# Kernel tuning notes

Measured on AMD Instinct MI355X. Metric: run time of the kernel, lower is better.

## Reference

```python
import jax, jax.numpy as jnp
import numpy as np

B, S, D = 1, 2048, 2048      # batch, seq, hidden_dim
DF = 768                      # moe intermediate (per routed expert)
DSH = 2048                    # shared-expert intermediate
E, K = 32, 8                  # num routed experts, top_k
BLK = 128                     # fp8 block-scale size
CAP = 1024
T = B * S


def _dequant(w, s, blk=BLK):
    # w: [E, M, N] fp8 values (stored fp32), s: [E, M/blk, N/blk] block scales
    Eh, M, N = w.shape
    Mb, Nb = s.shape[1], s.shape[2]
    return (w.reshape(Eh, Mb, blk, Nb, blk) * s[:, :, None, :, None]).reshape(Eh, M, N)


def setup_inputs() -> dict:
    key = jax.random.key(0)
    ks = jax.random.split(key, 13)
    n = lambda k, shp, sc=0.02: jax.random.normal(k, shp, jnp.float32) * sc
    u = lambda k, shp: jax.random.uniform(k, shp, jnp.float32, 0.005, 0.02)
    return {
        "hidden_states": jax.random.normal(ks[0], (B, S, D), jnp.float32),
        "router_w": n(ks[1], (E, D)),
        # raw fp8-value weights (simulated as fp32 integers-in-range values) + block scale_inv
        "wg_fp8": jax.random.normal(ks[2], (E, DF, D), jnp.float32),
        "sg": u(ks[3], (E, DF // BLK, D // BLK)),
        "wu_fp8": jax.random.normal(ks[4], (E, DF, D), jnp.float32),
        "su": u(ks[5], (E, DF // BLK, D // BLK)),
        "wd_fp8": jax.random.normal(ks[6], (E, D, DF), jnp.float32),
        "sd": u(ks[7], (E, D // BLK, DF // BLK)),
        "ws_gate": n(ks[8], (DSH, D)),
        "ws_up": n(ks[9], (DSH, D)),
        "ws_down": n(ks[10], (D, DSH)),
        "w_shared_gate": n(ks[11], (1, D)),
    }


def reference(hidden_states, router_w, wg_fp8, sg, wu_fp8, su, wd_fp8, sd,
              ws_gate, ws_up, ws_down, w_shared_gate):
    x = hidden_states.reshape(-1, D)  # [T, D]

    # shared expert (SwiGLU) + its sigmoid gate
    shared = (jax.nn.silu(x @ ws_gate.T) * (x @ ws_up.T)) @ ws_down.T
    sh_gate = jax.nn.sigmoid(x @ w_shared_gate.T)  # [T, 1]

    # router: softmax -> top-k -> renormalize (Qwen MoE gate)
    probs = jax.nn.softmax(x @ router_w.T, axis=-1)          # [T, E]
    rw, sel = jax.lax.top_k(probs, K)                        # [T, K]
    rw = rw / jnp.sum(rw, axis=-1, keepdims=True)

    # capacity-based dispatch (replaces the python per-expert loop; same math)
    flat_e = sel.reshape(-1)                                 # [T*K]
    oh = jax.nn.one_hot(flat_e, E, dtype=jnp.int32)
    pos = jnp.sum(jnp.cumsum(oh, axis=0) * oh, axis=-1) - 1  # position within expert
    keep = (pos < CAP)
    pos_c = jnp.minimum(pos, CAP)                            # overflow -> scratch slot CAP
    tok = jnp.arange(T * K) // K                             # owning token of each (t,k) pair

    buf = jnp.zeros((E, CAP + 1, D), x.dtype).at[flat_e, pos_c].set(x[tok])

    # block-scale dequant (fp8*scale_inv), then per-expert SwiGLU
    Wg = _dequant(wg_fp8, sg)
    Wu = _dequant(wu_fp8, su)
    Wd = _dequant(wd_fp8, sd)
    g = jnp.einsum('ecd,efd->ecf', buf, Wg)
    up = jnp.einsum('ecd,efd->ecf', buf, Wu)
    h = jax.nn.silu(g) * up
    y = jnp.einsum('ecf,edf->ecd', h, Wd)                    # [E, CAP+1, D]

    # weighted scatter-add back to tokens (index_add_ equivalent)
    y_tok = y[flat_e, pos_c]                                 # [T*K, D]
    w_tok = rw.reshape(-1) * keep.astype(x.dtype)
    out = jax.ops.segment_sum(y_tok * w_tok[:, None], tok, num_segments=T)

    out = out + sh_gate * shared
    return out.reshape(B, S, D)
```

## Files before the change

### kernel.cpp

```cpp
#include <hip/hip_runtime.h>
#include <hip/hip_bf16.h>


#define TT   2048
#define DD   2048
#define DFF  768
#define DSH  2048
#define EE   32
#define KTOP 8
#define CAP  1024

typedef _Float16 half8  __attribute__((ext_vector_type(8)));
typedef _Float16 half4v __attribute__((ext_vector_type(4)));
typedef float    f32x4  __attribute__((ext_vector_type(4)));

__global__ __launch_bounds__(256) void k_init(int* __restrict__ cnt,
                                              int* __restrict__ slot_tok) {
  int i = blockIdx.x * 256 + threadIdx.x;
  if (i < EE * CAP) slot_tok[i] = 0;
  if (i < EE) cnt[i] = 0;
}

__global__ __launch_bounds__(256) void k_cast(const float* __restrict__ in,
                                              _Float16* __restrict__ out) {
  int i = blockIdx.x * 256 + threadIdx.x;
  float4 v = ((const float4*)in)[i];
  half4v h = { (_Float16)v.x, (_Float16)v.y, (_Float16)v.z, (_Float16)v.w };
  ((half4v*)out)[i] = h;
}

template<int NCOLS>
__global__ void k_deq_row(const float* __restrict__ w, const float* __restrict__ s,
                          int mRows, _Float16* __restrict__ outp) {
  int r = blockIdx.x, e = blockIdx.y;
  int c4 = threadIdx.x;
  long long base = ((long long)e * mRows + r) * NCOLS;
  float sc = s[(e * (mRows >> 7) + (r >> 7)) * (NCOLS >> 7) + (c4 >> 5)];
  float4 v = ((const float4*)(w + base))[c4];
  half4v h = { (_Float16)(v.x * sc), (_Float16)(v.y * sc),
               (_Float16)(v.z * sc), (_Float16)(v.w * sc) };
  ((half4v*)(outp + base))[c4] = h;
}

__global__ __launch_bounds__(64) void k_router(
    const float* __restrict__ x, const float* __restrict__ rw,
    const float* __restrict__ wshg,
    float* __restrict__ shg, int* __restrict__ cnt,
    int* __restrict__ slot_tok, float* __restrict__ slot_w,
    int* __restrict__ slot_pair, int* __restrict__ pair_pos) {
  int t = blockIdx.x;
  int lane = threadIdx.x;
  const float* xr = x + (size_t)t * DD;
  float xv[32];
#pragma unroll
  for (int j = 0; j < 32; ++j) xv[j] = xr[lane + j * 64];

  __shared__ float lg[EE];
  for (int e = 0; e < EE; ++e) {
    const float* we = rw + (size_t)e * DD;
    float s = 0.f;
#pragma unroll
    for (int j = 0; j < 32; ++j) s += xv[j] * we[lane + j * 64];
#pragma unroll
    for (int off = 32; off > 0; off >>= 1) s += __shfl_down(s, off);
    if (lane == 0) lg[e] = s;
  }
  {
    float s = 0.f;
#pragma unroll
    for (int j = 0; j < 32; ++j) s += xv[j] * wshg[lane + j * 64];
#pragma unroll
    for (int off = 32; off > 0; off >>= 1) s += __shfl_down(s, off);
    if (lane == 0) shg[t] = 1.f / (1.f + expf(-s));
  }
  if (lane == 0) {
    unsigned used = 0;
    int sel[KTOP];
    float val[KTOP];
    for (int k = 0; k < KTOP; ++k) {
      float bv = -1e30f; int bi = 0;
      for (int e = 0; e < EE; ++e)
        if (!((used >> e) & 1) && lg[e] > bv) { bv = lg[e]; bi = e; }
      used |= (1u << bi);
      sel[k] = bi; val[k] = bv;
    }
    float mx = val[0], sum = 0.f;
    for (int k = 0; k < KTOP; ++k) { val[k] = expf(val[k] - mx); sum += val[k]; }
    float inv = 1.f / sum;
    for (int k = 0; k < KTOP; ++k) {
      int e = sel[k];
      int pos = atomicAdd(&cnt[e], 1);
      pair_pos[t * KTOP + k] = pos;
      if (pos < CAP) {
        slot_tok[e * CAP + pos] = t;
        slot_w[e * CAP + pos] = val[k] * inv;
        slot_pair[e * CAP + pos] = t * KTOP + k;
      }
    }
  }
}

template<bool DUAL, bool GATHER, int EPI, int NPB, int MBB, int KDIM>
__global__ __launch_bounds__(256, 2) void k_gemm16(
    const _Float16* __restrict__ A,
    const _Float16* __restrict__ B0h, const _Float16* __restrict__ B1h,
    _Float16* __restrict__ OutH, float* __restrict__ OutF,
    const float* __restrict__ shg,
    int ldA, int ldOut,
    long long strideAE, long long strideBE, long long strideOE,
    const int* __restrict__ cnt, int rowsConst,
    const int* __restrict__ slot_tok, const float* __restrict__ slot_w) {
  constexpr int BK = 64;
  constexpr int KT = KDIM / BK;
  constexpr int NF = DUAL ? 2 : 4;
  constexpr int BN = DUAL ? 64 : 128;

  const int f = blockIdx.x;
  const int xcd = f & 7;
  const int t0 = f >> 3;
  const int mb = t0 % MBB;
  const int pp = t0 / MBB;
  const int p  = pp * 8 + xcd;
  const int nb = p % NPB;
  const int e  = p / NPB;

  int rows = cnt ? (cnt[e] > CAP ? CAP : cnt[e]) : rowsConst;
  const int rowBase = mb * 128;
  if (rowBase >= rows) return;
  const int nBase = nb * BN;

  const int tid = threadIdx.x;
  const int lane = tid & 63;
  const int wave = tid >> 6;
  const int wr = wave >> 1;
  const int wc = wave & 1;

  __shared__ __align__(16) _Float16 sA[3][8192];
  __shared__ __align__(16) _Float16 sB[2][8192];

  const _Float16* Ae = A + (GATHER ? 0 : (long long)e * strideAE);
  const _Float16* B0e = B0h + (long long)e * strideBE;
  const _Float16* B1e = DUAL ? (B1h + (long long)e * strideBE) : nullptr;

  int aByte[4];
#pragma unroll
  for (int i = 0; i < 4; ++i) {
    int c = tid + i * 256;
    int row = c >> 3;
    int colB = ((c & 7) << 4) ^ ((row & 7) << 4);
    int src = GATHER ? slot_tok[e * CAP + rowBase + row] : (rowBase + row);
    aByte[i] = src * (2 * ldA) + colB;
  }
  int bByte[4];
#pragma unroll
  for (int i = 0; i < 4; ++i) {
    int c = tid + i * 256;
    int rn = DUAL ? ((c & 511) >> 3) : (c >> 3);
    int colB = ((c & 7) << 4) ^ ((rn & 7) << 4);
    bByte[i] = (nBase + rn) * (2 * KDIM) + colB;
  }

  f32x4 accG[4][NF];
  f32x4 accU[DUAL ? 4 : 1][NF];
#pragma unroll
  for (int m = 0; m < 4; ++m)
#pragma unroll
    for (int n = 0; n < NF; ++n) {
      accG[m][n] = (f32x4){0.f, 0.f, 0.f, 0.f};
      if constexpr (DUAL) accU[m][n] = (f32x4){0.f, 0.f, 0.f, 0.f};
    }

  auto stageA = [&](int kt, int buf) {
#pragma unroll
    for (int i = 0; i < 4; ++i) {
      __builtin_amdgcn_global_load_lds(
          (const __attribute__((address_space(1))) void*)
              ((const char*)Ae + aByte[i] + kt * 128),
          (__attribute__((address_space(3))) void*)&sA[buf][(tid + i * 256) * 8],
          16, 0, 0);
    }
  };
  auto stageB = [&](int kt, int buf) {
#pragma unroll
    for (int i = 0; i < 4; ++i) {
      const _Float16* src = (DUAL && i >= 2) ? B1e : B0e;
      __builtin_amdgcn_global_load_lds(
          (const __attribute__((address_space(1))) void*)
              ((const char*)src + bByte[i] + kt * 128),
          (__attribute__((address_space(3))) void*)&sB[buf][(tid + i * 256) * 8],
          16, 0, 0);
    }
  };
  auto computeTile = [&](int ia, int ib) {
    const char* pA = (const char*)&sA[ia][0];
    const char* pB = (const char*)&sB[ib][0];
#pragma unroll
    for (int kk = 0; kk < 2; ++kk) {
      const int koff = kk * 32 + (lane >> 4) * 8;
      half8 a[4];
#pragma unroll
      for (int m = 0; m < 4; ++m) {
        int r = wr * 64 + m * 16 + (lane & 15);
        int byt = ((r << 7) + (koff << 1)) ^ ((r & 7) << 4);
        a[m] = *(const half8*)(pA + byt);
      }
      if constexpr (DUAL) {
        half8 bg[2], bu[2];
#pragma unroll
        for (int n = 0; n < 2; ++n) {
          int rn = wc * 32 + n * 16 + (lane & 15);
          int byt = ((rn << 7) + (koff << 1)) ^ ((rn & 7) << 4);
          bg[n] = *(const half8*)(pB + byt);
          bu[n] = *(const half8*)(pB + 8192 + byt);
        }
#pragma unroll
        for (int m = 0; m < 4; ++m)
#pragma unroll
          for (int n = 0; n < 2; ++n) {
            accG[m][n] = __builtin_amdgcn_mfma_f32_16x16x32_f16(a[m], bg[n], accG[m][n], 0, 0, 0);
            accU[m][n] = __builtin_amdgcn_mfma_f32_16x16x32_f16(a[m], bu[n], accU[m][n], 0, 0, 0);
          }
      } else {
        half8 b[4];
#pragma unroll
        for (int n = 0; n < 4; ++n) {
          int rn = wc * 64 + n * 16 + (lane & 15);
          int byt = ((rn << 7) + (koff << 1)) ^ ((rn & 7) << 4);
          b[n] = *(const half8*)(pB + byt);
        }
#pragma unroll
        for (int m = 0; m < 4; ++m)
#pragma unroll
          for (int n = 0; n < 4; ++n)
            accG[m][n] = __builtin_amdgcn_mfma_f32_16x16x32_f16(a[m], b[n], accG[m][n], 0, 0, 0);
      }
    }
  };

  stageB(0, 0);
  __builtin_amdgcn_sched_barrier(0);
  stageA(0, 0);
  __builtin_amdgcn_sched_barrier(0);
  stageA(1, 1);
  __builtin_amdgcn_sched_barrier(0);

  int bufC = 0, bufW = 2;
  for (int kt = 0; kt < KT; ++kt) {
    asm volatile("s_waitcnt lgkmcnt(0)" ::: "memory");
    if (kt + 1 < KT) { asm volatile("s_waitcnt vmcnt(4)" ::: "memory"); }
    else             { asm volatile("s_waitcnt vmcnt(0)" ::: "memory"); }
    __builtin_amdgcn_sched_barrier(0);
    __builtin_amdgcn_s_barrier();
    __builtin_amdgcn_sched_barrier(0);
    if (kt + 1 < KT) stageB(kt + 1, (kt + 1) & 1);
    if (kt + 2 < KT) stageA(kt + 2, bufW);
    __builtin_amdgcn_sched_barrier(0);
    computeTile(bufC, kt & 1);
    bufC = (bufC == 2) ? 0 : bufC + 1;
    bufW = (bufW == 2) ? 0 : bufW + 1;
  }

#pragma unroll
  for (int m = 0; m < 4; ++m) {
#pragma unroll
    for (int i = 0; i < 4; ++i) {
      int row = rowBase + wr * 64 + m * 16 + (lane >> 4) * 4 + i;
      if (row < rows) {
        if constexpr (EPI == 1) {
          int pair = slot_tok[e * CAP + row];
          float w = slot_w[e * CAP + row];
#pragma unroll
          for (int n = 0; n < NF; ++n) {
            int col = nBase + wc * 64 + n * 16 + (lane & 15);
            OutH[(long long)pair * DD + col] = (_Float16)(w * accG[m][n][i]);
          }
        } else if constexpr (EPI == 2) {
          float g = shg[row];
#pragma unroll
          for (int n = 0; n < NF; ++n) {
            int col = nBase + wc * 64 + n * 16 + (lane & 15);
            OutF[(long long)row * DD + col] += g * accG[m][n][i];
          }
        } else {
          long long outBase = (long long)e * strideOE;
#pragma unroll
          for (int n = 0; n < NF; ++n) {
            int col = nBase + (DUAL ? wc * 32 : wc * 64) + n * 16 + (lane & 15);
            long long o = outBase + (long long)row * ldOut + col;
            if constexpr (DUAL) {
              float gv = accG[m][n][i];
              float uv = accU[m][n][i];
              OutH[o] = (_Float16)((gv / (1.f + __expf(-gv))) * uv);
            } else {
              OutH[o] = (_Float16)accG[m][n][i];
            }
          }
        }
      }
    }
  }
}

template<bool DUAL, bool GATHER, bool DEQ, int EPI, int NPB, int MBB, int KDIM>
__global__ __launch_bounds__(256, 2) void k_gemm(
    const _Float16* __restrict__ A,
    const float* __restrict__ B0f, const float* __restrict__ B1f,
    const float* __restrict__ S0, const float* __restrict__ S1,
    int sCols, int sStrideE,
    _Float16* __restrict__ OutH, float* __restrict__ OutF,
    const float* __restrict__ shg,
    int ldA, int ldOut,
    long long strideAE, long long strideBE, long long strideOE,
    const int* __restrict__ cnt, int rowsConst,
    const int* __restrict__ slot_tok, const float* __restrict__ slot_w) {
  constexpr int BK = 64;
  constexpr int KT = KDIM / BK;
  constexpr int NF = DUAL ? 2 : 4;
  constexpr int BN = DUAL ? 64 : 128;
  constexpr int BCH = DUAL ? 4 : 8;

  const int f = blockIdx.x;
  const int xcd = f & 7;
  const int t0 = f >> 3;
  const int mb = t0 % MBB;
  const int pp = t0 / MBB;
  const int p  = pp * 8 + xcd;
  const int nb = p % NPB;
  const int e  = p / NPB;

  int rows = cnt ? (cnt[e] > CAP ? CAP : cnt[e]) : rowsConst;
  const int rowBase = mb * 128;
  if (rowBase >= rows) return;
  const int nBase = nb * BN;

  const int tid = threadIdx.x;
  const int lane = tid & 63;
  const int wave = tid >> 6;
  const int wr = wave >> 1;
  const int wc = wave & 1;

  __shared__ __align__(16) _Float16 sA[3][8192];
  __shared__ __align__(16) _Float16 sB[2][8192];

  const _Float16* Ae = A + (GATHER ? 0 : (long long)e * strideAE);
  const float* B0e = B0f + (long long)e * strideBE;
  const float* B1e = DUAL ? (B1f + (long long)e * strideBE) : nullptr;
  const float* S0e = DEQ ? (S0 + (long long)e * sStrideE) : nullptr;
  const float* S1e = (DEQ && DUAL) ? (S1 + (long long)e * sStrideE) : nullptr;
  const int sRow = DEQ ? (nBase >> 7) * sCols : 0;

  int aByte[4];
#pragma unroll
  for (int i = 0; i < 4; ++i) {
    int c = tid + i * 256;
    int row = c >> 3;
    int colB = ((c & 7) << 4) ^ ((row & 7) << 4);
    int src = GATHER ? slot_tok[e * CAP + rowBase + row] : (rowBase + row);
    aByte[i] = src * (2 * ldA) + colB;
  }
  int bOff[BCH], wByte[BCH];
#pragma unroll
  for (int i = 0; i < BCH; ++i) {
    int c = tid + i * 256;
    int rn = c >> 4;
    int c4 = (c & 15) << 2;
    bOff[i] = (nBase + rn) * KDIM + c4;
    wByte[i] = ((rn << 7) + (c4 << 1)) ^ ((rn & 7) << 4);
  }

  f32x4 accG[4][NF];
  f32x4 accU[DUAL ? 4 : 1][NF];
#pragma unroll
  for (int m = 0; m < 4; ++m)
#pragma unroll
    for (int n = 0; n < NF; ++n) {
      accG[m][n] = (f32x4){0.f, 0.f, 0.f, 0.f};
      if constexpr (DUAL) accU[m][n] = (f32x4){0.f, 0.f, 0.f, 0.f};
    }

  auto stageA = [&](int kt, int buf) {
#pragma unroll
    for (int i = 0; i < 4; ++i) {
      __builtin_amdgcn_global_load_lds(
          (const __attribute__((address_space(1))) void*)
              ((const char*)Ae + aByte[i] + kt * (BK * 2)),
          (__attribute__((address_space(3))) void*)&sA[buf][(tid + i * 256) * 8],
          16, 0, 0);
    }
  };
  auto loadB = [&](int kt, float4 (&r0)[BCH], float4 (&r1)[BCH]) {
    const int ko = kt * BK;
#pragma unroll
    for (int i = 0; i < BCH; ++i) r0[i] = *(const float4*)(B0e + bOff[i] + ko);
    if constexpr (DUAL) {
#pragma unroll
      for (int i = 0; i < BCH; ++i) r1[i] = *(const float4*)(B1e + bOff[i] + ko);
    }
  };
  auto storeB = [&](int kt, float4 (&r0)[BCH], float4 (&r1)[BCH]) {
    float s0 = 1.f, s1 = 1.f;
    if constexpr (DEQ) {
      s0 = S0e[sRow + (kt >> 1)];
      if constexpr (DUAL) s1 = S1e[sRow + (kt >> 1)];
    }
    char* base = (char*)&sB[kt & 1][0];
#pragma unroll
    for (int i = 0; i < BCH; ++i) {
      half4v h = { (_Float16)(r0[i].x * s0), (_Float16)(r0[i].y * s0),
                   (_Float16)(r0[i].z * s0), (_Float16)(r0[i].w * s0) };
      *(half4v*)(base + wByte[i]) = h;
      if constexpr (DUAL) {
        half4v h1 = { (_Float16)(r1[i].x * s1), (_Float16)(r1[i].y * s1),
                      (_Float16)(r1[i].z * s1), (_Float16)(r1[i].w * s1) };
        *(half4v*)(base + 8192 + wByte[i]) = h1;
      }
    }
  };
  auto computeTile = [&](int ia, int ib) {
    const char* pA = (const char*)&sA[ia][0];
    const char* pB = (const char*)&sB[ib][0];
#pragma unroll
    for (int kk = 0; kk < 2; ++kk) {
      const int koff = kk * 32 + (lane >> 4) * 8;
      half8 a[4];
#pragma unroll
      for (int m = 0; m < 4; ++m) {
        int r = wr * 64 + m * 16 + (lane & 15);
        int byt = ((r << 7) + (koff << 1)) ^ ((r & 7) << 4);
        a[m] = *(const half8*)(pA + byt);
      }
      if constexpr (DUAL) {
        half8 bg[2], bu[2];
#pragma unroll
        for (int n = 0; n < 2; ++n) {
          int rn = wc * 32 + n * 16 + (lane & 15);
          int byt = ((rn << 7) + (koff << 1)) ^ ((rn & 7) << 4);
          bg[n] = *(const half8*)(pB + byt);
          bu[n] = *(const half8*)(pB + 8192 + byt);
        }
#pragma unroll
        for (int m = 0; m < 4; ++m)
#pragma unroll
          for (int n = 0; n < 2; ++n) {
            accG[m][n] = __builtin_amdgcn_mfma_f32_16x16x32_f16(a[m], bg[n], accG[m][n], 0, 0, 0);
            accU[m][n] = __builtin_amdgcn_mfma_f32_16x16x32_f16(a[m], bu[n], accU[m][n], 0, 0, 0);
          }
      } else {
        half8 b[4];
#pragma unroll
        for (int n = 0; n < 4; ++n) {
          int rn = wc * 64 + n * 16 + (lane & 15);
          int byt = ((rn << 7) + (koff << 1)) ^ ((rn & 7) << 4);
          b[n] = *(const half8*)(pB + byt);
        }
#pragma unroll
        for (int m = 0; m < 4; ++m)
#pragma unroll
          for (int n = 0; n < 4; ++n)
            accG[m][n] = __builtin_amdgcn_mfma_f32_16x16x32_f16(a[m], b[n], accG[m][n], 0, 0, 0);
      }
    }
  };

  float4 rbE0[BCH], rbE1[BCH], rbO0[BCH], rbO1[BCH];

  stageA(0, 0); loadB(0, rbE0, rbE1);
  __builtin_amdgcn_sched_barrier(0);
  stageA(1, 1); loadB(1, rbO0, rbO1);
  __builtin_amdgcn_sched_barrier(0);

  int bufC = 0, bufW = 2;

  for (int kt = 0; kt < KT; kt += 2) {
    if (kt + 1 < KT) { asm volatile("s_waitcnt vmcnt(12)" ::: "memory"); }
    else             { asm volatile("s_waitcnt vmcnt(0)"  ::: "memory"); }
    __builtin_amdgcn_sched_barrier(0);
    storeB(kt, rbE0, rbE1);
    asm volatile("s_waitcnt lgkmcnt(0)" ::: "memory");
    __builtin_amdgcn_sched_barrier(0);
    __builtin_amdgcn_s_barrier();
    __builtin_amdgcn_sched_barrier(0);
    if (kt + 2 < KT) { stageA(kt + 2, bufW); loadB(kt + 2, rbE0, rbE1); }
    __builtin_amdgcn_sched_barrier(0);
    computeTile(bufC, 0);
    bufC = (bufC == 2) ? 0 : bufC + 1;
    bufW = (bufW == 2) ? 0 : bufW + 1;

    if (kt + 2 < KT) { asm volatile("s_waitcnt vmcnt(12)" ::: "memory"); }
    else             { asm volatile("s_waitcnt vmcnt(0)"  ::: "memory"); }
    __builtin_amdgcn_sched_barrier(0);
    storeB(kt + 1, rbO0, rbO1);
    asm volatile("s_waitcnt lgkmcnt(0)" ::: "memory");
    __builtin_amdgcn_sched_barrier(0);
    __builtin_amdgcn_s_barrier();
    __builtin_amdgcn_sched_barrier(0);
    if (kt + 3 < KT) { stageA(kt + 3, bufW); loadB(kt + 3, rbO0, rbO1); }
    __builtin_amdgcn_sched_barrier(0);
    computeTile(bufC, 1);
    bufC = (bufC == 2) ? 0 : bufC + 1;
    bufW = (bufW == 2) ? 0 : bufW + 1;
  }

#pragma unroll
  for (int m = 0; m < 4; ++m) {
#pragma unroll
    for (int i = 0; i < 4; ++i) {
      int row = rowBase + wr * 64 + m * 16 + (lane >> 4) * 4 + i;
      if (row < rows) {
        if constexpr (EPI == 1) {
          int pair = slot_tok[e * CAP + row];
          float w = slot_w[e * CAP + row];
#pragma unroll
          for (int n = 0; n < NF; ++n) {
            int col = nBase + wc * 64 + n * 16 + (lane & 15);
            OutH[(long long)pair * DD + col] = (_Float16)(w * accG[m][n][i]);
          }
        } else if constexpr (EPI == 2) {
          float g = shg[row];
#pragma unroll
          for (int n = 0; n < NF; ++n) {
            int col = nBase + wc * 64 + n * 16 + (lane & 15);
            OutF[(long long)row * DD + col] += g * accG[m][n][i];
          }
        } else {
          long long outBase = (long long)e * strideOE;
#pragma unroll
          for (int n = 0; n < NF; ++n) {
            int col = nBase + (DUAL ? wc * 32 : wc * 64) + n * 16 + (lane & 15);
            long long o = outBase + (long long)row * ldOut + col;
            if constexpr (DUAL) {
              float gv = accG[m][n][i];
              float uv = accU[m][n][i];
              OutH[o] = (_Float16)((gv / (1.f + __expf(-gv))) * uv);
            } else {
              OutH[o] = (_Float16)accG[m][n][i];
            }
          }
        }
      }
    }
  }
}

__global__ __launch_bounds__(256) void k_combine(
    const _Float16* __restrict__ Yp, const int* __restrict__ pair_pos,
    float* __restrict__ out) {
  int t = blockIdx.x;
  int col = threadIdx.x * 8;
  float acc[8] = {0.f, 0.f, 0.f, 0.f, 0.f, 0.f, 0.f, 0.f};
#pragma unroll
  for (int k = 0; k < KTOP; ++k) {
    if (pair_pos[t * KTOP + k] < CAP) {
      half8 y = *(const half8*)&Yp[((size_t)t * KTOP + k) * DD + col];
#pragma unroll
      for (int j = 0; j < 8; ++j) acc[j] += (float)y[j];
    }
  }
  float4 o0 = {acc[0], acc[1], acc[2], acc[3]};
  float4 o1 = {acc[4], acc[5], acc[6], acc[7]};
  *(float4*)&out[(size_t)t * DD + col] = o0;
  *(float4*)&out[(size_t)t * DD + col + 4] = o1;
}

extern "C" void kernel_launch(void* const* d_in, const int* in_sizes, int n_in,
                              void* d_out, int out_size, void* d_ws, size_t ws_size,
                              hipStream_t stream) {
  (void)in_sizes; (void)n_in; (void)out_size;
  const float* x    = (const float*)d_in[0];
  const float* rw   = (const float*)d_in[1];
  const float* wg   = (const float*)d_in[2];
  const float* sg   = (const float*)d_in[3];
  const float* wu   = (const float*)d_in[4];
  const float* su   = (const float*)d_in[5];
  const float* wd   = (const float*)d_in[6];
  const float* sd   = (const float*)d_in[7];
  const float* wsg  = (const float*)d_in[8];
  const float* wsu  = (const float*)d_in[9];
  const float* wsd  = (const float*)d_in[10];
  const float* wshg = (const float*)d_in[11];
  float* out = (float*)d_out;

  char* p = (char*)d_ws;
  auto alloc = [&](size_t bytes) {
    char* r = p;
    p += (bytes + 255) & ~(size_t)255;
    return r;
  };

  const bool big = ws_size >= (size_t)270 * 1000 * 1000;

  if (big) {
    _Float16* x_h  = (_Float16*)alloc((size_t)TT * DD * 2);
    _Float16* bufA = (_Float16*)alloc((size_t)EE * DFF * DD * 2);
    _Float16* bufB = (_Float16*)alloc((size_t)EE * DFF * DD * 2);
    _Float16* bufH = (_Float16*)alloc((size_t)EE * CAP * DFF * 2);
    _Float16* Hsh  = (_Float16*)alloc((size_t)TT * DSH * 2);
    float* shg     = (float*)alloc((size_t)TT * 4);
    int* cnt       = (int*)alloc((size_t)EE * 4);
    int* slot_tok  = (int*)alloc((size_t)EE * CAP * 4);
    float* slot_w  = (float*)alloc((size_t)EE * CAP * 4);
    int* slot_pair = (int*)alloc((size_t)EE * CAP * 4);
    int* pair_pos  = (int*)alloc((size_t)TT * KTOP * 4);

    _Float16* Yp    = bufB;
    _Float16* wsg_h = bufH;
    _Float16* wsu_h = bufH + (size_t)TT * DD;
    _Float16* wsd_h = bufH + (size_t)2 * TT * DD;

    k_init<<<(EE * CAP + 255) / 256, 256, 0, stream>>>(cnt, slot_tok);
    k_cast<<<(TT * DD / 4) / 256, 256, 0, stream>>>(x, x_h);
    k_router<<<TT, 64, 0, stream>>>(x, rw, wshg, shg, cnt, slot_tok, slot_w,
                                    slot_pair, pair_pos);

    k_deq_row<DD><<<dim3(DFF, EE), DD / 4, 0, stream>>>(wg, sg, DFF, bufA);
    k_deq_row<DD><<<dim3(DFF, EE), DD / 4, 0, stream>>>(wu, su, DFF, bufB);

    k_gemm16<true, true, 0, 12, 8, DD><<<3072, 256, 0, stream>>>(
        x_h, bufA, bufB, bufH, nullptr, nullptr,
        DD, DFF, 0LL, (long long)DFF * DD, (long long)CAP * DFF,
        cnt, 0, slot_tok, nullptr);

    k_deq_row<DFF><<<dim3(DD, EE), DFF / 4, 0, stream>>>(wd, sd, DD, bufA);
    k_gemm16<false, false, 1, 16, 8, DFF><<<4096, 256, 0, stream>>>(
        bufH, bufA, bufA, Yp, nullptr, nullptr,
        DFF, DD, (long long)CAP * DFF, (long long)DD * DFF, 0LL,
        cnt, 0, slot_pair, slot_w);

    k_combine<<<TT, 256, 0, stream>>>(Yp, pair_pos, out);

    k_cast<<<(DD * DSH / 4) / 256, 256, 0, stream>>>(wsg, wsg_h);
    k_cast<<<(DD * DSH / 4) / 256, 256, 0, stream>>>(wsu, wsu_h);
    k_cast<<<(DD * DSH / 4) / 256, 256, 0, stream>>>(wsd, wsd_h);

    k_gemm16<true, false, 0, 32, 16, DD><<<512, 256, 0, stream>>>(
        x_h, wsg_h, wsu_h, Hsh, nullptr, nullptr,
        DD, DSH, 0LL, 0LL, 0LL,
        nullptr, TT, nullptr, nullptr);

    k_gemm16<false, false, 2, 16, 16, DSH><<<256, 256, 0, stream>>>(
        Hsh, wsd_h, wsd_h, nullptr, out, shg,
        DSH, DD, 0LL, 0LL, 0LL,
        nullptr, TT, nullptr, nullptr);
  } else {
    _Float16* x_h   = (_Float16*)alloc((size_t)TT * DD * 2);
    _Float16* H     = (_Float16*)alloc((size_t)EE * CAP * DFF * 2);
    _Float16* Hsh   = (_Float16*)alloc((size_t)TT * DSH * 2);
    _Float16* Yp    = (_Float16*)alloc((size_t)TT * KTOP * DD * 2);
    float* shg      = (float*)alloc((size_t)TT * 4);
    int* cnt        = (int*)alloc((size_t)EE * 4);
    int* slot_tok   = (int*)alloc((size_t)EE * CAP * 4);
    float* slot_w   = (float*)alloc((size_t)EE * CAP * 4);
    int* slot_pair  = (int*)alloc((size_t)EE * CAP * 4);
    int* pair_pos   = (int*)alloc((size_t)TT * KTOP * 4);

    k_init<<<(EE * CAP + 255) / 256, 256, 0, stream>>>(cnt, slot_tok);
    k_cast<<<(TT * DD / 4) / 256, 256, 0, stream>>>(x, x_h);
    k_router<<<TT, 64, 0, stream>>>(x, rw, wshg, shg, cnt, slot_tok, slot_w,
                                    slot_pair, pair_pos);

    k_gemm<true, true, true, 0, 12, 8, DD><<<3072, 256, 0, stream>>>(
        x_h, wg, wu, sg, su, DD / 128, (DFF / 128) * (DD / 128),
        H, nullptr, nullptr,
        DD, DFF, 0LL, (long long)DFF * DD, (long long)CAP * DFF,
        cnt, 0, slot_tok, nullptr);

    k_gemm<false, false, true, 1, 16, 8, DFF><<<4096, 256, 0, stream>>>(
        H, wd, wd, sd, sd, DFF / 128, (DD / 128) * (DFF / 128),
        Yp, nullptr, nullptr,
        DFF, DD, (long long)CAP * DFF, (long long)DD * DFF, 0LL,
        cnt, 0, slot_pair, slot_w);

    k_combine<<<TT, 256, 0, stream>>>(Yp, pair_pos, out);

    k_gemm<true, false, false, 0, 32, 16, DD><<<512, 256, 0, stream>>>(
        x_h, wsg, wsu, nullptr, nullptr, 0, 0,
        Hsh, nullptr, nullptr,
        DD, DSH, 0LL, 0LL, 0LL,
        nullptr, TT, nullptr, nullptr);

    k_gemm<false, false, false, 2, 16, 16, DSH><<<256, 256, 0, stream>>>(
        Hsh, wsd, wsd, nullptr, nullptr, 0, 0,
        nullptr, out, shg,
        DSH, DD, 0LL, 0LL, 0LL,
        nullptr, TT, nullptr, nullptr);
  }
}
```

Before: 747.3 us.

## Fuse routed-expert weight dequant into GEMM and drop the precomputed-weight path

Removes the workspace-size switch and the separate dequant kernels that wrote fp16 copies of the expert weights. The routed-expert GEMMs now read fp32 fp8-valued weights and block scales directly, scaling and converting them in registers before writing to LDS. Shared-expert weights are always cast to fp16 up front and use the plain fp16 GEMM. This saves the full write and re-read of the dequantized expert weights. In exchange, each M-block re-reads fp32 weights and does the conversion inside the GEMM loop, which puts more pressure on L2 and registers.

```diff
diff --git a/kernel.cpp b/kernel.cpp
--- a/kernel.cpp
+++ b/kernel.cpp
@@ -27,19 +27,6 @@
   float4 v = ((const float4*)in)[i];
   half4v h = { (_Float16)v.x, (_Float16)v.y, (_Float16)v.z, (_Float16)v.w };
   ((half4v*)out)[i] = h;
-}
-
-template<int NCOLS>
-__global__ void k_deq_row(const float* __restrict__ w, const float* __restrict__ s,
-                          int mRows, _Float16* __restrict__ outp) {
-  int r = blockIdx.x, e = blockIdx.y;
-  int c4 = threadIdx.x;
-  long long base = ((long long)e * mRows + r) * NCOLS;
-  float sc = s[(e * (mRows >> 7) + (r >> 7)) * (NCOLS >> 7) + (c4 >> 5)];
-  float4 v = ((const float4*)(w + base))[c4];
-  half4v h = { (_Float16)(v.x * sc), (_Float16)(v.y * sc),
-               (_Float16)(v.z * sc), (_Float16)(v.w * sc) };
-  ((half4v*)(outp + base))[c4] = h;
 }
 
 __global__ __launch_bounds__(64) void k_router(
@@ -101,19 +88,21 @@
 }
 
 template<bool DUAL, bool GATHER, int EPI, int NPB, int MBB, int KDIM>
-__global__ __launch_bounds__(256, 2) void k_gemm16(
+__global__ __launch_bounds__(256, 2) void k_gemm(
     const _Float16* __restrict__ A,
-    const _Float16* __restrict__ B0h, const _Float16* __restrict__ B1h,
-    _Float16* __restrict__ OutH, float* __restrict__ OutF,
-    const float* __restrict__ shg,
+    const float* __restrict__ B0f, const float* __restrict__ B1f,
+    const float* __restrict__ S0, const float* __restrict__ S1,
+    int sCols, int sStrideE,
+    _Float16* __restrict__ OutH,
     int ldA, int ldOut,
     long long strideAE, long long strideBE, long long strideOE,
-    const int* __restrict__ cnt, int rowsConst,
+    const int* __restrict__ cnt,
     const int* __restrict__ slot_tok, const float* __restrict__ slot_w) {
   constexpr int BK = 64;
   constexpr int KT = KDIM / BK;
   constexpr int NF = DUAL ? 2 : 4;
   constexpr int BN = DUAL ? 64 : 128;
+  constexpr int BCH = DUAL ? 4 : 8;
 
   const int f = blockIdx.x;
   const int xcd = f & 7;
@@ -124,7 +113,7 @@
   const int nb = p % NPB;
   const int e  = p / NPB;
 
-  int rows = cnt ? (cnt[e] > CAP ? CAP : cnt[e]) : rowsConst;
+  int rows = cnt[e] > CAP ? CAP : cnt[e];
   const int rowBase = mb * 128;
   if (rowBase >= rows) return;
   const int nBase = nb * BN;
@@ -139,8 +128,11 @@
   __shared__ __align__(16) _Float16 sB[2][8192];
 
   const _Float16* Ae = A + (GATHER ? 0 : (long long)e * strideAE);
-  const _Float16* B0e = B0h + (long long)e * strideBE;
-  const _Float16* B1e = DUAL ? (B1h + (long long)e * strideBE) : nullptr;
+  const float* B0e = B0f + (long long)e * strideBE;
+  const float* B1e = DUAL ? (B1f + (long long)e * strideBE) : nullptr;
+  const float* S0e = S0 + (long long)e * sStrideE;
+  const float* S1e = DUAL ? (S1 + (long long)e * sStrideE) : nullptr;
+  const int sRow = (nBase >> 7) * sCols;
 
   int aByte[4];
 #pragma unroll
@@ -151,6 +143,218 @@
     int src = GATHER ? slot_tok[e * CAP + rowBase + row] : (rowBase + row);
     aByte[i] = src * (2 * ldA) + colB;
   }
+  int bOff[BCH], wByte[BCH];
+#pragma unroll
+  for (int i = 0; i < BCH; ++i) {
+    int c = tid + i * 256;
+    int rn = c >> 4;
+    int c4 = (c & 15) << 2;
+    bOff[i] = (nBase + rn) * KDIM + c4;
+    wByte[i] = ((rn << 7) + (c4 << 1)) ^ ((rn & 7) << 4);
+  }
+
+  f32x4 accG[4][NF];
+  f32x4 accU[DUAL ? 4 : 1][NF];
+#pragma unroll
+  for (int m = 0; m < 4; ++m)
+#pragma unroll
+    for (int n = 0; n < NF; ++n) {
+      accG[m][n] = (f32x4){0.f, 0.f, 0.f, 0.f};
+      if constexpr (DUAL) accU[m][n] = (f32x4){0.f, 0.f, 0.f, 0.f};
+    }
+
+  auto stageA = [&](int kt, int buf) {
+#pragma unroll
+    for (int i = 0; i < 4; ++i) {
+      __builtin_amdgcn_global_load_lds(
+          (const __attribute__((address_space(1))) void*)
+              ((const char*)Ae + aByte[i] + kt * (BK * 2)),
+          (__attribute__((address_space(3))) void*)&sA[buf][(tid + i * 256) * 8],
+          16, 0, 0);
+    }
+  };
+  auto loadB = [&](int kt, float4 (&r0)[BCH], float4 (&r1)[BCH]) {
+    const int ko = kt * BK;
+#pragma unroll
+    for (int i = 0; i < BCH; ++i) r0[i] = *(const float4*)(B0e + bOff[i] + ko);
+    if constexpr (DUAL) {
+#pragma unroll
+      for (int i = 0; i < BCH; ++i) r1[i] = *(const float4*)(B1e + bOff[i] + ko);
+    }
+  };
+  auto storeB = [&](int kt, float4 (&r0)[BCH], float4 (&r1)[BCH]) {
+    float s0 = S0e[sRow + (kt >> 1)];
+    float s1 = DUAL ? S1e[sRow + (kt >> 1)] : 0.f;
+    char* base = (char*)&sB[kt & 1][0];
+#pragma unroll
+    for (int i = 0; i < BCH; ++i) {
+      half4v h = { (_Float16)(r0[i].x * s0), (_Float16)(r0[i].y * s0),
+                   (_Float16)(r0[i].z * s0), (_Float16)(r0[i].w * s0) };
+      *(half4v*)(base + wByte[i]) = h;
+      if constexpr (DUAL) {
+        half4v h1 = { (_Float16)(r1[i].x * s1), (_Float16)(r1[i].y * s1),
+                      (_Float16)(r1[i].z * s1), (_Float16)(r1[i].w * s1) };
+        *(half4v*)(base + 8192 + wByte[i]) = h1;
+      }
+    }
+  };
+  auto computeTile = [&](int ia, int ib) {
+    const char* pA = (const char*)&sA[ia][0];
+    const char* pB = (const char*)&sB[ib][0];
+#pragma unroll
+    for (int kk = 0; kk < 2; ++kk) {
+      const int koff = kk * 32 + (lane >> 4) * 8;
+      half8 a[4];
+#pragma unroll
+      for (int m = 0; m < 4; ++m) {
+        int r = wr * 64 + m * 16 + (lane & 15);
+        int byt = ((r << 7) + (koff << 1)) ^ ((r & 7) << 4);
+        a[m] = *(const half8*)(pA + byt);
+      }
+      if constexpr (DUAL) {
+        half8 bg[2], bu[2];
+#pragma unroll
+        for (int n = 0; n < 2; ++n) {
+          int rn = wc * 32 + n * 16 + (lane & 15);
+          int byt = ((rn << 7) + (koff << 1)) ^ ((rn & 7) << 4);
+          bg[n] = *(const half8*)(pB + byt);
+          bu[n] = *(const half8*)(pB + 8192 + byt);
+        }
+#pragma unroll
+        for (int m = 0; m < 4; ++m)
+#pragma unroll
+          for (int n = 0; n < 2; ++n) {
+            accG[m][n] = __builtin_amdgcn_mfma_f32_16x16x32_f16(a[m], bg[n], accG[m][n], 0, 0, 0);
+            accU[m][n] = __builtin_amdgcn_mfma_f32_16x16x32_f16(a[m], bu[n], accU[m][n], 0, 0, 0);
+          }
+      } else {
+        half8 b[4];
+#pragma unroll
+        for (int n = 0; n < 4; ++n) {
+          int rn = wc * 64 + n * 16 + (lane & 15);
+          int byt = ((rn << 7) + (koff << 1)) ^ ((rn & 7) << 4);
+          b[n] = *(const half8*)(pB + byt);
+        }
+#pragma unroll
+        for (int m = 0; m < 4; ++m)
+#pragma unroll
+          for (int n = 0; n < 4; ++n)
+            accG[m][n] = __builtin_amdgcn_mfma_f32_16x16x32_f16(a[m], b[n], accG[m][n], 0, 0, 0);
+      }
+    }
+  };
+
+  float4 rbE0[BCH], rbE1[BCH], rbO0[BCH], rbO1[BCH];
+
+  loadB(0, rbE0, rbE1);
+  loadB(1, rbO0, rbO1);
+  stageA(0, 0);
+  stageA(1, 1);
+  __builtin_amdgcn_sched_barrier(0);
+  storeB(0, rbE0, rbE1);
+  asm volatile("s_waitcnt lgkmcnt(0)" ::: "memory");
+  asm volatile("s_waitcnt vmcnt(4)" ::: "memory");
+  __builtin_amdgcn_s_barrier();
+  __builtin_amdgcn_sched_barrier(0);
+
+  int bufC = 0, bufW = 2;
+  for (int kt = 0; kt < KT; ++kt) {
+    if (kt + 2 < KT) {
+      stageA(kt + 2, bufW);
+      if (kt & 1) loadB(kt + 2, rbO0, rbO1);
+      else        loadB(kt + 2, rbE0, rbE1);
+      __builtin_amdgcn_sched_barrier(0);
+    }
+    computeTile(bufC, kt & 1);
+    if (kt + 1 < KT) {
+      if (kt & 1) storeB(kt + 1, rbE0, rbE1);
+      else        storeB(kt + 1, rbO0, rbO1);
+    }
+    asm volatile("s_waitcnt lgkmcnt(0)" ::: "memory");
+    if (kt + 2 < KT) { asm volatile("s_waitcnt vmcnt(12)" ::: "memory"); }
+    else             { asm volatile("s_waitcnt vmcnt(0)"  ::: "memory"); }
+    __builtin_amdgcn_s_barrier();
+    __builtin_amdgcn_sched_barrier(0);
+    bufC = (bufC == 2) ? 0 : bufC + 1;
+    bufW = (bufW == 2) ? 0 : bufW + 1;
+  }
+
+#pragma unroll
+  for (int m = 0; m < 4; ++m) {
+#pragma unroll
+    for (int i = 0; i < 4; ++i) {
+      int row = rowBase + wr * 64 + m * 16 + (lane >> 4) * 4 + i;
+      if (row < rows) {
+        if constexpr (EPI == 1) {
+          int pair = slot_tok[e * CAP + row];
+          float w = slot_w[e * CAP + row];
+#pragma unroll
+          for (int n = 0; n < NF; ++n) {
+            int col = nBase + wc * 64 + n * 16 + (lane & 15);
+            OutH[(long long)pair * DD + col] = (_Float16)(w * accG[m][n][i]);
+          }
+        } else {
+          long long outBase = (long long)e * strideOE;
+#pragma unroll
+          for (int n = 0; n < NF; ++n) {
+            int col = nBase + (DUAL ? wc * 32 : wc * 64) + n * 16 + (lane & 15);
+            long long o = outBase + (long long)row * ldOut + col;
+            if constexpr (DUAL) {
+              float gv = accG[m][n][i];
+              float uv = accU[m][n][i];
+              OutH[o] = (_Float16)((gv / (1.f + __expf(-gv))) * uv);
+            } else {
+              OutH[o] = (_Float16)accG[m][n][i];
+            }
+          }
+        }
+      }
+    }
+  }
+}
+
+template<bool DUAL, int EPI, int NPB, int MBB, int KDIM>
+__global__ __launch_bounds__(256, 2) void k_gemm16(
+    const _Float16* __restrict__ A,
+    const _Float16* __restrict__ B0h, const _Float16* __restrict__ B1h,
+    _Float16* __restrict__ OutH, float* __restrict__ OutF,
+    const float* __restrict__ shg,
+    int ldA, int ldOut, int rowsConst) {
+  constexpr int BK = 64;
+  constexpr int KT = KDIM / BK;
+  constexpr int NF = DUAL ? 2 : 4;
+  constexpr int BN = DUAL ? 64 : 128;
+
+  const int f = blockIdx.x;
+  const int xcd = f & 7;
+  const int t0 = f >> 3;
+  const int mb = t0 % MBB;
+  const int pp = t0 / MBB;
+  const int p  = pp * 8 + xcd;
+  const int nb = p % NPB;
+
+  int rows = rowsConst;
+  const int rowBase = mb * 128;
+  if (rowBase >= rows) return;
+  const int nBase = nb * BN;
+
+  const int tid = threadIdx.x;
+  const int lane = tid & 63;
+  const int wave = tid >> 6;
+  const int wr = wave >> 1;
+  const int wc = wave & 1;
+
+  __shared__ __align__(16) _Float16 sA[3][8192];
+  __shared__ __align__(16) _Float16 sB[2][8192];
+
+  int aByte[4];
+#pragma unroll
+  for (int i = 0; i < 4; ++i) {
+    int c = tid + i * 256;
+    int row = c >> 3;
+    int colB = ((c & 7) << 4) ^ ((row & 7) << 4);
+    aByte[i] = (rowBase + row) * (2 * ldA) + colB;
+  }
   int bByte[4];
 #pragma unroll
   for (int i = 0; i < 4; ++i) {
@@ -175,7 +379,7 @@
     for (int i = 0; i < 4; ++i) {
       __builtin_amdgcn_global_load_lds(
           (const __attribute__((address_space(1))) void*)
-              ((const char*)Ae + aByte[i] + kt * 128),
+              ((const char*)A + aByte[i] + kt * 128),
           (__attribute__((address_space(3))) void*)&sA[buf][(tid + i * 256) * 8],
           16, 0, 0);
     }
@@ -183,7 +387,7 @@
   auto stageB = [&](int kt, int buf) {
 #pragma unroll
     for (int i = 0; i < 4; ++i) {
-      const _Float16* src = (DUAL && i >= 2) ? B1e : B0e;
+      const _Float16* src = (DUAL && i >= 2) ? B1h : B0h;
       __builtin_amdgcn_global_load_lds(
           (const __attribute__((address_space(1))) void*)
               ((const char*)src + bByte[i] + kt * 128),
@@ -266,15 +470,7 @@
     for (int i = 0; i < 4; ++i) {
       int row = rowBase + wr * 64 + m * 16 + (lane >> 4) * 4 + i;
       if (row < rows) {
-        if constexpr (EPI == 1) {
-          int pair = slot_tok[e * CAP + row];
-          float w = slot_w[e * CAP + row];
-#pragma unroll
-          for (int n = 0; n < NF; ++n) {
-            int col = nBase + wc * 64 + n * 16 + (lane & 15);
-            OutH[(long long)pair * DD + col] = (_Float16)(w * accG[m][n][i]);
-          }
-        } else if constexpr (EPI == 2) {
+        if constexpr (EPI == 2) {
           float g = shg[row];
 #pragma unroll
           for (int n = 0; n < NF; ++n) {
@@ -282,11 +478,10 @@
             OutF[(long long)row * DD + col] += g * accG[m][n][i];
           }
         } else {
-          long long outBase = (long long)e * strideOE;
 #pragma unroll
           for (int n = 0; n < NF; ++n) {
             int col = nBase + (DUAL ? wc * 32 : wc * 64) + n * 16 + (lane & 15);
-            long long o = outBase + (long long)row * ldOut + col;
+            long long o = (long long)row * ldOut + col;
             if constexpr (DUAL) {
               float gv = accG[m][n][i];
               float uv = accU[m][n][i];
@@ -301,247 +496,6 @@
   }
 }
 
-template<bool DUAL, bool GATHER, bool DEQ, int EPI, int NPB, int MBB, int KDIM>
-__global__ __launch_bounds__(256, 2) void k_gemm(
-    const _Float16* __restrict__ A,
-    const float* __restrict__ B0f, const float* __restrict__ B1f,
-    const float* __restrict__ S0, const float* __restrict__ S1,
-    int sCols, int sStrideE,
-    _Float16* __restrict__ OutH, float* __restrict__ OutF,
-    const float* __restrict__ shg,
-    int ldA, int ldOut,
-    long long strideAE, long long strideBE, long long strideOE,
-    const int* __restrict__ cnt, int rowsConst,
-    const int* __restrict__ slot_tok, const float* __restrict__ slot_w) {
-  constexpr int BK = 64;
-  constexpr int KT = KDIM / BK;
-  constexpr int NF = DUAL ? 2 : 4;
-  constexpr int BN = DUAL ? 64 : 128;
-  constexpr int BCH = DUAL ? 4 : 8;
-
-  const int f = blockIdx.x;
-  const int xcd = f & 7;
-  const int t0 = f >> 3;
-  const int mb = t0 % MBB;
-  const int pp = t0 / MBB;
-  const int p  = pp * 8 + xcd;
-  const int nb = p % NPB;
-  const int e  = p / NPB;
-
-  int rows = cnt ? (cnt[e] > CAP ? CAP : cnt[e]) : rowsConst;
-  const int rowBase = mb * 128;
-  if (rowBase >= rows) return;
-  const int nBase = nb * BN;
-
-  const int tid = threadIdx.x;
-  const int lane = tid & 63;
-  const int wave = tid >> 6;
-  const int wr = wave >> 1;
-  const int wc = wave & 1;
-
-  __shared__ __align__(16) _Float16 sA[3][8192];
-  __shared__ __align__(16) _Float16 sB[2][8192];
-
-  const _Float16* Ae = A + (GATHER ? 0 : (long long)e * strideAE);
-  const float* B0e = B0f + (long long)e * strideBE;
-  const float* B1e = DUAL ? (B1f + (long long)e * strideBE) : nullptr;
-  const float* S0e = DEQ ? (S0 + (long long)e * sStrideE) : nullptr;
-  const float* S1e = (DEQ && DUAL) ? (S1 + (long long)e * sStrideE) : nullptr;
-  const int sRow = DEQ ? (nBase >> 7) * sCols : 0;
-
-  int aByte[4];
-#pragma unroll
-  for (int i = 0; i < 4; ++i) {
-    int c = tid + i * 256;
-    int row = c >> 3;
-    int colB = ((c & 7) << 4) ^ ((row & 7) << 4);
-    int src = GATHER ? slot_tok[e * CAP + rowBase + row] : (rowBase + row);
-    aByte[i] = src * (2 * ldA) + colB;
-  }
-  int bOff[BCH], wByte[BCH];
-#pragma unroll
-  for (int i = 0; i < BCH; ++i) {
-    int c = tid + i * 256;
-    int rn = c >> 4;
-    int c4 = (c & 15) << 2;
-    bOff[i] = (nBase + rn) * KDIM + c4;
-    wByte[i] = ((rn << 7) + (c4 << 1)) ^ ((rn & 7) << 4);
-  }
-
-  f32x4 accG[4][NF];
-  f32x4 accU[DUAL ? 4 : 1][NF];
-#pragma unroll
-  for (int m = 0; m < 4; ++m)
-#pragma unroll
-    for (int n = 0; n < NF; ++n) {
-      accG[m][n] = (f32x4){0.f, 0.f, 0.f, 0.f};
-      if constexpr (DUAL) accU[m][n] = (f32x4){0.f, 0.f, 0.f, 0.f};
-    }
-
-  auto stageA = [&](int kt, int buf) {
-#pragma unroll
-    for (int i = 0; i < 4; ++i) {
-      __builtin_amdgcn_global_load_lds(
-          (const __attribute__((address_space(1))) void*)
-              ((const char*)Ae + aByte[i] + kt * (BK * 2)),
-          (__attribute__((address_space(3))) void*)&sA[buf][(tid + i * 256) * 8],
-          16, 0, 0);
-    }
-  };
-  auto loadB = [&](int kt, float4 (&r0)[BCH], float4 (&r1)[BCH]) {
-    const int ko = kt * BK;
-#pragma unroll
-    for (int i = 0; i < BCH; ++i) r0[i] = *(const float4*)(B0e + bOff[i] + ko);
-    if constexpr (DUAL) {
-#pragma unroll
-      for (int i = 0; i < BCH; ++i) r1[i] = *(const float4*)(B1e + bOff[i] + ko);
-    }
-  };
-  auto storeB = [&](int kt, float4 (&r0)[BCH], float4 (&r1)[BCH]) {
-    float s0 = 1.f, s1 = 1.f;
-    if constexpr (DEQ) {
-      s0 = S0e[sRow + (kt >> 1)];
-      if constexpr (DUAL) s1 = S1e[sRow + (kt >> 1)];
-    }
-    char* base = (char*)&sB[kt & 1][0];
-#pragma unroll
-    for (int i = 0; i < BCH; ++i) {
-      half4v h = { (_Float16)(r0[i].x * s0), (_Float16)(r0[i].y * s0),
-                   (_Float16)(r0[i].z * s0), (_Float16)(r0[i].w * s0) };
-      *(half4v*)(base + wByte[i]) = h;
-      if constexpr (DUAL) {
-        half4v h1 = { (_Float16)(r1[i].x * s1), (_Float16)(r1[i].y * s1),
-                      (_Float16)(r1[i].z * s1), (_Float16)(r1[i].w * s1) };
-        *(half4v*)(base + 8192 + wByte[i]) = h1;
-      }
-    }
-  };
-  auto computeTile = [&](int ia, int ib) {
-    const char* pA = (const char*)&sA[ia][0];
-    const char* pB = (const char*)&sB[ib][0];
-#pragma unroll
-    for (int kk = 0; kk < 2; ++kk) {
-      const int koff = kk * 32 + (lane >> 4) * 8;
-      half8 a[4];
-#pragma unroll
-      for (int m = 0; m < 4; ++m) {
-        int r = wr * 64 + m * 16 + (lane & 15);
-        int byt = ((r << 7) + (koff << 1)) ^ ((r & 7) << 4);
-        a[m] = *(const half8*)(pA + byt);
-      }
-      if constexpr (DUAL) {
-        half8 bg[2], bu[2];
-#pragma unroll
-        for (int n = 0; n < 2; ++n) {
-          int rn = wc * 32 + n * 16 + (lane & 15);
-          int byt = ((rn << 7) + (koff << 1)) ^ ((rn & 7) << 4);
-          bg[n] = *(const half8*)(pB + byt);
-          bu[n] = *(const half8*)(pB + 8192 + byt);
-        }
-#pragma unroll
-        for (int m = 0; m < 4; ++m)
-#pragma unroll
-          for (int n = 0; n < 2; ++n) {
-            accG[m][n] = __builtin_amdgcn_mfma_f32_16x16x32_f16(a[m], bg[n], accG[m][n], 0, 0, 0);
-            accU[m][n] = __builtin_amdgcn_mfma_f32_16x16x32_f16(a[m], bu[n], accU[m][n], 0, 0, 0);
-          }
-      } else {
-        half8 b[4];
-#pragma unroll
-        for (int n = 0; n < 4; ++n) {
-          int rn = wc * 64 + n * 16 + (lane & 15);
-          int byt = ((rn << 7) + (koff << 1)) ^ ((rn & 7) << 4);
-          b[n] = *(const half8*)(pB + byt);
-        }
-#pragma unroll
-        for (int m = 0; m < 4; ++m)
-#pragma unroll
-          for (int n = 0; n < 4; ++n)
-            accG[m][n] = __builtin_amdgcn_mfma_f32_16x16x32_f16(a[m], b[n], accG[m][n], 0, 0, 0);
-      }
-    }
-  };
-
-  float4 rbE0[BCH], rbE1[BCH], rbO0[BCH], rbO1[BCH];
-
-  stageA(0, 0); loadB(0, rbE0, rbE1);
-  __builtin_amdgcn_sched_barrier(0);
-  stageA(1, 1); loadB(1, rbO0, rbO1);
-  __builtin_amdgcn_sched_barrier(0);
-
-  int bufC = 0, bufW = 2;
-
-  for (int kt = 0; kt < KT; kt += 2) {
-    if (kt + 1 < KT) { asm volatile("s_waitcnt vmcnt(12)" ::: "memory"); }
-    else             { asm volatile("s_waitcnt vmcnt(0)"  ::: "memory"); }
-    __builtin_amdgcn_sched_barrier(0);
-    storeB(kt, rbE0, rbE1);
-    asm volatile("s_waitcnt lgkmcnt(0)" ::: "memory");
-    __builtin_amdgcn_sched_barrier(0);
-    __builtin_amdgcn_s_barrier();
-    __builtin_amdgcn_sched_barrier(0);
-    if (kt + 2 < KT) { stageA(kt + 2, bufW); loadB(kt + 2, rbE0, rbE1); }
-    __builtin_amdgcn_sched_barrier(0);
-    computeTile(bufC, 0);
-    bufC = (bufC == 2) ? 0 : bufC + 1;
-    bufW = (bufW == 2) ? 0 : bufW + 1;
-
-    if (kt + 2 < KT) { asm volatile("s_waitcnt vmcnt(12)" ::: "memory"); }
-    else             { asm volatile("s_waitcnt vmcnt(0)"  ::: "memory"); }
-    __builtin_amdgcn_sched_barrier(0);
-    storeB(kt + 1, rbO0, rbO1);
-    asm volatile("s_waitcnt lgkmcnt(0)" ::: "memory");
-    __builtin_amdgcn_sched_barrier(0);
-    __builtin_amdgcn_s_barrier();
-    __builtin_amdgcn_sched_barrier(0);
-    if (kt + 3 < KT) { stageA(kt + 3, bufW); loadB(kt + 3, rbO0, rbO1); }
-    __builtin_amdgcn_sched_barrier(0);
-    computeTile(bufC, 1);
-    bufC = (bufC == 2) ? 0 : bufC + 1;
-    bufW = (bufW == 2) ? 0 : bufW + 1;
-  }
-
-#pragma unroll
-  for (int m = 0; m < 4; ++m) {
-#pragma unroll
-    for (int i = 0; i < 4; ++i) {
-      int row = rowBase + wr * 64 + m * 16 + (lane >> 4) * 4 + i;
-      if (row < rows) {
-        if constexpr (EPI == 1) {
-          int pair = slot_tok[e * CAP + row];
-          float w = slot_w[e * CAP + row];
-#pragma unroll
-          for (int n = 0; n < NF; ++n) {
-            int col = nBase + wc * 64 + n * 16 + (lane & 15);
-            OutH[(long long)pair * DD + col] = (_Float16)(w * accG[m][n][i]);
-          }
-        } else if constexpr (EPI == 2) {
-          float g = shg[row];
-#pragma unroll
-          for (int n = 0; n < NF; ++n) {
-            int col = nBase + wc * 64 + n * 16 + (lane & 15);
-            OutF[(long long)row * DD + col] += g * accG[m][n][i];
-          }
-        } else {
-          long long outBase = (long long)e * strideOE;
-#pragma unroll
-          for (int n = 0; n < NF; ++n) {
-            int col = nBase + (DUAL ? wc * 32 : wc * 64) + n * 16 + (lane & 15);
-            long long o = outBase + (long long)row * ldOut + col;
-            if constexpr (DUAL) {
-              float gv = accG[m][n][i];
-              float uv = accU[m][n][i];
-              OutH[o] = (_Float16)((gv / (1.f + __expf(-gv))) * uv);
-            } else {
-              OutH[o] = (_Float16)accG[m][n][i];
-            }
-          }
-        }
-      }
-    }
-  }
-}
-
 __global__ __launch_bounds__(256) void k_combine(
     const _Float16* __restrict__ Yp, const int* __restrict__ pair_pos,
     float* __restrict__ out) {
@@ -565,7 +519,7 @@
 extern "C" void kernel_launch(void* const* d_in, const int* in_sizes, int n_in,
                               void* d_out, int out_size, void* d_ws, size_t ws_size,
                               hipStream_t stream) {
-  (void)in_sizes; (void)n_in; (void)out_size;
+  (void)in_sizes; (void)n_in; (void)out_size; (void)ws_size;
   const float* x    = (const float*)d_in[0];
   const float* rw   = (const float*)d_in[1];
   const float* wg   = (const float*)d_in[2];
@@ -586,102 +540,47 @@
     p += (bytes + 255) & ~(size_t)255;
     return r;
   };
-
-  const bool big = ws_size >= (size_t)270 * 1000 * 1000;
-
-  if (big) {
-    _Float16* x_h  = (_Float16*)alloc((size_t)TT * DD * 2);
-    _Float16* bufA = (_Float16*)alloc((size_t)EE * DFF * DD * 2);
-    _Float16* bufB = (_Float16*)alloc((size_t)EE * DFF * DD * 2);
-    _Float16* bufH = (_Float16*)alloc((size_t)EE * CAP * DFF * 2);
-    _Float16* Hsh  = (_Float16*)alloc((size_t)TT * DSH * 2);
-    float* shg     = (float*)alloc((size_t)TT * 4);
-    int* cnt       = (int*)alloc((size_t)EE * 4);
-    int* slot_tok  = (int*)alloc((size_t)EE * CAP * 4);
-    float* slot_w  = (float*)alloc((size_t)EE * CAP * 4);
-    int* slot_pair = (int*)alloc((size_t)EE * CAP * 4);
-    int* pair_pos  = (int*)alloc((size_t)TT * KTOP * 4);
-
-    _Float16* Yp    = bufB;
-    _Float16* wsg_h = bufH;
-    _Float16* wsu_h = bufH + (size_t)TT * DD;
-    _Float16* wsd_h = bufH + (size_t)2 * TT * DD;
-
-    k_init<<<(EE * CAP + 255) / 256, 256, 0, stream>>>(cnt, slot_tok);
-    k_cast<<<(TT * DD / 4) / 256, 256, 0, stream>>>(x, x_h);
-    k_router<<<TT, 64, 0, stream>>>(x, rw, wshg, shg, cnt, slot_tok, slot_w,
-                                    slot_pair, pair_pos);
-
-    k_deq_row<DD><<<dim3(DFF, EE), DD / 4, 0, stream>>>(wg, sg, DFF, bufA);
-    k_deq_row<DD><<<dim3(DFF, EE), DD / 4, 0, stream>>>(wu, su, DFF, bufB);
-
-    k_gemm16<true, true, 0, 12, 8, DD><<<3072, 256, 0, stream>>>(
-        x_h, bufA, bufB, bufH, nullptr, nullptr,
-        DD, DFF, 0LL, (long long)DFF * DD, (long long)CAP * DFF,
-        cnt, 0, slot_tok, nullptr);
-
-    k_deq_row<DFF><<<dim3(DD, EE), DFF / 4, 0, stream>>>(wd, sd, DD, bufA);
-    k_gemm16<false, false, 1, 16, 8, DFF><<<4096, 256, 0, stream>>>(
-        bufH, bufA, bufA, Yp, nullptr, nullptr,
-        DFF, DD, (long long)CAP * DFF, (long long)DD * DFF, 0LL,
-        cnt, 0, slot_pair, slot_w);
-
-    k_combine<<<TT, 256, 0, stream>>>(Yp, pair_pos, out);
-
-    k_cast<<<(DD * DSH / 4) / 256, 256, 0, stream>>>(wsg, wsg_h);
-    k_cast<<<(DD * DSH / 4) / 256, 256, 0, stream>>>(wsu, wsu_h);
-    k_cast<<<(DD * DSH / 4) / 256, 256, 0, stream>>>(wsd, wsd_h);
-
-    k_gemm16<true, false, 0, 32, 16, DD><<<512, 256, 0, stream>>>(
-        x_h, wsg_h, wsu_h, Hsh, nullptr, nullptr,
-        DD, DSH, 0LL, 0LL, 0LL,
-        nullptr, TT, nullptr, nullptr);
-
-    k_gemm16<false, false, 2, 16, 16, DSH><<<256, 256, 0, stream>>>(
-        Hsh, wsd_h, wsd_h, nullptr, out, shg,
-        DSH, DD, 0LL, 0LL, 0LL,
-        nullptr, TT, nullptr, nullptr);
-  } else {
-    _Float16* x_h   = (_Float16*)alloc((size_t)TT * DD * 2);
-    _Float16* H     = (_Float16*)alloc((size_t)EE * CAP * DFF * 2);
-    _Float16* Hsh   = (_Float16*)alloc((size_t)TT * DSH * 2);
-    _Float16* Yp    = (_Float16*)alloc((size_t)TT * KTOP * DD * 2);
-    float* shg      = (float*)alloc((size_t)TT * 4);
-    int* cnt        = (int*)alloc((size_t)EE * 4);
-    int* slot_tok   = (int*)alloc((size_t)EE * CAP * 4);
-    float* slot_w   = (float*)alloc((size_t)EE * CAP * 4);
-    int* slot_pair  = (int*)alloc((size_t)EE * CAP * 4);
-    int* pair_pos   = (int*)alloc((size_t)TT * KTOP * 4);
-
-    k_init<<<(EE * CAP + 255) / 256, 256, 0, stream>>>(cnt, slot_tok);
-    k_cast<<<(TT * DD / 4) / 256, 256, 0, stream>>>(x, x_h);
-    k_router<<<TT, 64, 0, stream>>>(x, rw, wshg, shg, cnt, slot_tok, slot_w,
-                                    slot_pair, pair_pos);
-
-    k_gemm<true, true, true, 0, 12, 8, DD><<<3072, 256, 0, stream>>>(
-        x_h, wg, wu, sg, su, DD / 128, (DFF / 128) * (DD / 128),
-        H, nullptr, nullptr,
-        DD, DFF, 0LL, (long long)DFF * DD, (long long)CAP * DFF,
-        cnt, 0, slot_tok, nullptr);
-
-    k_gemm<false, false, true, 1, 16, 8, DFF><<<4096, 256, 0, stream>>>(
-        H, wd, wd, sd, sd, DFF / 128, (DD / 128) * (DFF / 128),
-        Yp, nullptr, nullptr,
-        DFF, DD, (long long)CAP * DFF, (long long)DD * DFF, 0LL,
-        cnt, 0, slot_pair, slot_w);
-
-    k_combine<<<TT, 256, 0, stream>>>(Yp, pair_pos, out);
-
-    k_gemm<true, false, false, 0, 32, 16, DD><<<512, 256, 0, stream>>>(
-        x_h, wsg, wsu, nullptr, nullptr, 0, 0,
-        Hsh, nullptr, nullptr,
-        DD, DSH, 0LL, 0LL, 0LL,
-        nullptr, TT, nullptr, nullptr);
-
-    k_gemm<false, false, false, 2, 16, 16, DSH><<<256, 256, 0, stream>>>(
-        Hsh, wsd, wsd, nullptr, nullptr, 0, 0,
-        nullptr, out, shg,
-        DSH, DD, 0LL, 0LL, 0LL,
-        nullptr, TT, nullptr, nullptr);
-  }
-}
+  _Float16* x_h   = (_Float16*)alloc((size_t)TT * DD * 2);
+  _Float16* H     = (_Float16*)alloc((size_t)EE * CAP * DFF * 2);
+  _Float16* Hsh   = (_Float16*)alloc((size_t)TT * DSH * 2);
+  _Float16* Yp    = (_Float16*)alloc((size_t)TT * KTOP * DD * 2);
+  _Float16* wsg_h = (_Float16*)alloc((size_t)DSH * DD * 2);
+  _Float16* wsu_h = (_Float16*)alloc((size_t)DSH * DD * 2);
+  _Float16* wsd_h = (_Float16*)alloc((size_t)DD * DSH * 2);
+  float* shg      = (float*)alloc((size_t)TT * 4);
+  int* cnt        = (int*)alloc((size_t)EE * 4);
+  int* slot_tok   = (int*)alloc((size_t)EE * CAP * 4);
+  float* slot_w   = (float*)alloc((size_t)EE * CAP * 4);
+  int* slot_pair  = (int*)alloc((size_t)EE * CAP * 4);
+  int* pair_pos   = (int*)alloc((size_t)TT * KTOP * 4);
+
+  k_init<<<(EE * CAP + 255) / 256, 256, 0, stream>>>(cnt, slot_tok);
+  k_cast<<<(TT * DD / 4) / 256, 256, 0, stream>>>(x, x_h);
+  k_cast<<<(DSH * DD / 4) / 256, 256, 0, stream>>>(wsg, wsg_h);
+  k_cast<<<(DSH * DD / 4) / 256, 256, 0, stream>>>(wsu, wsu_h);
+  k_cast<<<(DD * DSH / 4) / 256, 256, 0, stream>>>(wsd, wsd_h);
+  k_router<<<TT, 64, 0, stream>>>(x, rw, wshg, shg, cnt, slot_tok, slot_w,
+                                  slot_pair, pair_pos);
+
+  k_gemm<true, true, 0, 12, 8, DD><<<3072, 256, 0, stream>>>(
+      x_h, wg, wu, sg, su, DD / 128, (DFF / 128) * (DD / 128),
+      H, DD, DFF,
+      0LL, (long long)DFF * DD, (long long)CAP * DFF,
+      cnt, slot_tok, nullptr);
+
+  k_gemm<false, false, 1, 16, 8, DFF><<<4096, 256, 0, stream>>>(
+      H, wd, wd, sd, sd, DFF / 128, (DD / 128) * (DFF / 128),
+      Yp, DFF, DD,
+      (long long)CAP * DFF, (long long)DD * DFF, 0LL,
+      cnt, slot_pair, slot_w);
+
+  k_combine<<<TT, 256, 0, stream>>>(Yp, pair_pos, out);
+
+  k_gemm16<true, 0, 32, 16, DD><<<512, 256, 0, stream>>>(
+      x_h, wsg_h, wsu_h, Hsh, nullptr, nullptr,
+      DD, DSH, TT);
+
+  k_gemm16<false, 2, 16, 16, DSH><<<256, 256, 0, stream>>>(
+      Hsh, wsd_h, wsd_h, nullptr, out, shg,
+      DSH, DD, TT);
+}
```

New measurement: 762.2 us. 1.02x slower.
